# Kernel tuning notes

Measured on AMD Instinct MI355X. Metric: run time of the kernel, lower is better.

## Reference

```python
import jax, jax.numpy as jnp
import numpy as np

TAU = 1.0

def setup_inputs() -> dict:
    key = jax.random.key(0)
    scores = jax.random.normal(key, (16, 2048), dtype=jnp.float32)
    return {"scores": scores}

def reference(scores) -> jnp.ndarray:
    # scores: [B, n]
    B, n = scores.shape
    s = scores[:, :, None]                                  # [B, n, 1]
    # pairwise abs differences |s_i - s_j|
    A = jnp.abs(s - jnp.swapaxes(s, 1, 2))                  # [B, n, n]
    # torch: matmul(matmul(A, ones), ones^T) == row-sums broadcast over cols
    Bsum = jnp.sum(A, axis=-1, keepdims=True)               # [B, n, 1]
    # scaling_j = n + 1 - 2*(j+1)
    scaling = (n + 1 - 2 * (jnp.arange(n) + 1)).astype(scores.dtype)  # [n]
    C = s * scaling[None, None, :]                          # [B, n, n]
    P_max = jnp.swapaxes(C - Bsum, 1, 2)                    # [B, n, n]
    P_hat = jax.nn.softmax(P_max / TAU, axis=-1)
    return P_hat
```

## Files before the change

### kernel.cpp

```cpp
#include <hip/hip_runtime.h>
#include <math.h>

#define N 2048
#define BATCH 16

__global__ __launch_bounds__(128) void bsum_kernel(const float* __restrict__ scores,
                                                   float* __restrict__ dsum) {
    __shared__ float s_sh[N];
    const int b = blockIdx.x >> 4;
    const int jBase = (blockIdx.x & 15) * 128;
    const float* s = scores + (size_t)b * N;

    for (int t = threadIdx.x; t < N / 4; t += 128) {
        ((float4*)s_sh)[t] = ((const float4*)s)[t];
    }
    __syncthreads();

    const int j = jBase + threadIdx.x;
    const float sj = s_sh[j];
    float acc = 0.f;
#pragma unroll 8
    for (int k = 0; k < N / 4; ++k) {
        float4 v = ((const float4*)s_sh)[k];
        acc += fabsf(sj - v.x) + fabsf(sj - v.y) + fabsf(sj - v.z) + fabsf(sj - v.w);
    }
    dsum[(size_t)b * N + j] = acc;
}

__global__ __launch_bounds__(256) void softmax_kernel(const float* __restrict__ scores,
                                                      const float* __restrict__ dsum,
                                                      float* __restrict__ out) {
    __shared__ float s_sh[N];
    __shared__ float d_sh[N];

    const int blocksPerBatch = N / 4;
    const int b = blockIdx.x / blocksPerBatch;
    const int blockRow = blockIdx.x % blocksPerBatch;

    const float* s = scores + (size_t)b * N;
    const float* dd = dsum + (size_t)b * N;

    for (int t = threadIdx.x; t < N / 4; t += 256) {
        ((float4*)s_sh)[t] = ((const float4*)s)[t];
        ((float4*)d_sh)[t] = ((const float4*)dd)[t];
    }
    __syncthreads();

    const int wave = threadIdx.x >> 6;
    const int lane = threadIdx.x & 63;
    const int row = blockRow * 4 + wave;
    const float c = (float)(N - 1 - 2 * row);

    float lg[32];
    float m = -INFINITY;
#pragma unroll
    for (int it = 0; it < 8; ++it) {
        const int idx = it * 64 + lane;
        float4 s4 = ((const float4*)s_sh)[idx];
        float4 d4 = ((const float4*)d_sh)[idx];
        float l0 = fmaf(c, s4.x, -d4.x);
        float l1 = fmaf(c, s4.y, -d4.y);
        float l2 = fmaf(c, s4.z, -d4.z);
        float l3 = fmaf(c, s4.w, -d4.w);
        lg[it * 4 + 0] = l0;
        lg[it * 4 + 1] = l1;
        lg[it * 4 + 2] = l2;
        lg[it * 4 + 3] = l3;
        m = fmaxf(m, fmaxf(fmaxf(l0, l1), fmaxf(l2, l3)));
    }
#pragma unroll
    for (int off = 32; off > 0; off >>= 1)
        m = fmaxf(m, __shfl_xor(m, off, 64));

    float sum = 0.f;
#pragma unroll
    for (int k = 0; k < 32; ++k) {
        lg[k] = __expf(lg[k] - m);
        sum += lg[k];
    }
#pragma unroll
    for (int off = 32; off > 0; off >>= 1)
        sum += __shfl_xor(sum, off, 64);

    const float inv = 1.0f / sum;

    float* orow = out + (((size_t)b * N) + row) * N;
#pragma unroll
    for (int it = 0; it < 8; ++it) {
        const int idx = it * 64 + lane;
        float4 o;
        o.x = lg[it * 4 + 0] * inv;
        o.y = lg[it * 4 + 1] * inv;
        o.z = lg[it * 4 + 2] * inv;
        o.w = lg[it * 4 + 3] * inv;
        ((float4*)orow)[idx] = o;
    }
}

extern "C" void kernel_launch(void* const* d_in, const int* in_sizes, int n_in,
                              void* d_out, int out_size, void* d_ws, size_t ws_size,
                              hipStream_t stream) {
    const float* scores = (const float*)d_in[0];
    float* out = (float*)d_out;
    float* dsum = (float*)d_ws;

    bsum_kernel<<<BATCH * 16, 128, 0, stream>>>(scores, dsum);
    softmax_kernel<<<BATCH * (N / 4), 256, 0, stream>>>(scores, dsum, out);
}
```

Baseline: 269.5 us.

## Process four rows per wave from registers with nontemporal output stores

```diff
diff --git a/kernel.cpp b/kernel.cpp
--- a/kernel.cpp
+++ b/kernel.cpp
@@ -3,6 +3,8 @@
 
 #define N 2048
 #define BATCH 16
+
+typedef float f32x4 __attribute__((ext_vector_type(4)));
 
 __global__ __launch_bounds__(128) void bsum_kernel(const float* __restrict__ scores,
                                                    float* __restrict__ dsum) {
@@ -30,70 +32,67 @@
 __global__ __launch_bounds__(256) void softmax_kernel(const float* __restrict__ scores,
                                                       const float* __restrict__ dsum,
                                                       float* __restrict__ out) {
-    __shared__ float s_sh[N];
-    __shared__ float d_sh[N];
+    const int waveId = blockIdx.x * 4 + (threadIdx.x >> 6);
+    const int lane = threadIdx.x & 63;
+    const int rowBase = waveId * 4;
+    const int b = rowBase >> 11;
+    const int i0 = rowBase & 2047;
 
-    const int blocksPerBatch = N / 4;
-    const int b = blockIdx.x / blocksPerBatch;
-    const int blockRow = blockIdx.x % blocksPerBatch;
+    const float4* s4p = (const float4*)(scores + (size_t)b * N);
+    const float4* d4p = (const float4*)(dsum + (size_t)b * N);
 
-    const float* s = scores + (size_t)b * N;
-    const float* dd = dsum + (size_t)b * N;
-
-    for (int t = threadIdx.x; t < N / 4; t += 256) {
-        ((float4*)s_sh)[t] = ((const float4*)s)[t];
-        ((float4*)d_sh)[t] = ((const float4*)dd)[t];
-    }
-    __syncthreads();
-
-    const int wave = threadIdx.x >> 6;
-    const int lane = threadIdx.x & 63;
-    const int row = blockRow * 4 + wave;
-    const float c = (float)(N - 1 - 2 * row);
-
-    float lg[32];
-    float m = -INFINITY;
+    float4 s4[8], d4[8];
 #pragma unroll
     for (int it = 0; it < 8; ++it) {
-        const int idx = it * 64 + lane;
-        float4 s4 = ((const float4*)s_sh)[idx];
-        float4 d4 = ((const float4*)d_sh)[idx];
-        float l0 = fmaf(c, s4.x, -d4.x);
-        float l1 = fmaf(c, s4.y, -d4.y);
-        float l2 = fmaf(c, s4.z, -d4.z);
-        float l3 = fmaf(c, s4.w, -d4.w);
-        lg[it * 4 + 0] = l0;
-        lg[it * 4 + 1] = l1;
-        lg[it * 4 + 2] = l2;
-        lg[it * 4 + 3] = l3;
-        m = fmaxf(m, fmaxf(fmaxf(l0, l1), fmaxf(l2, l3)));
+        s4[it] = s4p[it * 64 + lane];
+        d4[it] = d4p[it * 64 + lane];
     }
+
+#pragma unroll 1
+    for (int r = 0; r < 4; ++r) {
+        const int row = i0 + r;
+        const float c = (float)(N - 1 - 2 * row);
+
+        float lg[32];
+        float m = -INFINITY;
 #pragma unroll
-    for (int off = 32; off > 0; off >>= 1)
-        m = fmaxf(m, __shfl_xor(m, off, 64));
+        for (int it = 0; it < 8; ++it) {
+            float l0 = fmaf(c, s4[it].x, -d4[it].x);
+            float l1 = fmaf(c, s4[it].y, -d4[it].y);
+            float l2 = fmaf(c, s4[it].z, -d4[it].z);
+            float l3 = fmaf(c, s4[it].w, -d4[it].w);
+            lg[it * 4 + 0] = l0;
+            lg[it * 4 + 1] = l1;
+            lg[it * 4 + 2] = l2;
+            lg[it * 4 + 3] = l3;
+            m = fmaxf(m, fmaxf(fmaxf(l0, l1), fmaxf(l2, l3)));
+        }
+#pragma unroll
+        for (int off = 32; off > 0; off >>= 1)
+            m = fmaxf(m, __shfl_xor(m, off, 64));
 
-    float sum = 0.f;
+        float sum = 0.f;
 #pragma unroll
-    for (int k = 0; k < 32; ++k) {
-        lg[k] = __expf(lg[k] - m);
-        sum += lg[k];
-    }
+        for (int k = 0; k < 32; ++k) {
+            lg[k] = __expf(lg[k] - m);
+            sum += lg[k];
+        }
 #pragma unroll
-    for (int off = 32; off > 0; off >>= 1)
-        sum += __shfl_xor(sum, off, 64);
+        for (int off = 32; off > 0; off >>= 1)
+            sum += __shfl_xor(sum, off, 64);
 
-    const float inv = 1.0f / sum;
+        const float inv = 1.0f / sum;
 
-    float* orow = out + (((size_t)b * N) + row) * N;
+        f32x4* orow = (f32x4*)(out + (((size_t)b * N) + row) * N);
 #pragma unroll
-    for (int it = 0; it < 8; ++it) {
-        const int idx = it * 64 + lane;
-        float4 o;
-        o.x = lg[it * 4 + 0] * inv;
-        o.y = lg[it * 4 + 1] * inv;
-        o.z = lg[it * 4 + 2] * inv;
-        o.w = lg[it * 4 + 3] * inv;
-        ((float4*)orow)[idx] = o;
+        for (int it = 0; it < 8; ++it) {
+            f32x4 o;
+            o.x = lg[it * 4 + 0] * inv;
+            o.y = lg[it * 4 + 1] * inv;
+            o.z = lg[it * 4 + 2] * inv;
+            o.w = lg[it * 4 + 3] * inv;
+            __builtin_nontemporal_store(o, &orow[it * 64 + lane]);
+        }
     }
 }
 
@@ -105,5 +104,5 @@
     float* dsum = (float*)d_ws;
 
     bsum_kernel<<<BATCH * 16, 128, 0, stream>>>(scores, dsum);
-    softmax_kernel<<<BATCH * (N / 4), 256, 0, stream>>>(scores, dsum, out);
+    softmax_kernel<<<32768 / 16, 256, 0, stream>>>(scores, dsum, out);
 }
```

After: 277.5 us. +3.0%, slower.
